# Kernel optimization log

Hardware: AMD Instinct MI355X
Metric: run time of the kernel (lower is better)

Reference implementation:

```python
import jax, jax.numpy as jnp
import numpy as np

VOCAB = 32000
DIM = 1024
DEPTH = 4
SEQ = 512
HEADS = 16
NMB = 4
MAXMEM = NMB * SEQ  # 2048
RAMP = 128
COEF = 1e-06
B = 4
DH = DIM // HEADS


def _ln(x, g, b):
    mu = jnp.mean(x, axis=-1, keepdims=True)
    v = jnp.mean((x - mu) ** 2, axis=-1, keepdims=True)
    return (x - mu) / jnp.sqrt(v + 1e-5) * g + b


def setup_inputs() -> dict:
    key = jax.random.key(0)
    ks = jax.random.split(key, 24)
    s = 0.02
    inp = {
        'tokens': jax.random.randint(ks[0], (B, SEQ), 0, VOCAB),
        'mems': jax.random.normal(ks[1], (DEPTH, B, MAXMEM, DIM), jnp.float32) * s,
        'times': jax.random.randint(ks[2], (DEPTH, MAXMEM), 0, 4096, dtype=jnp.int32),
        'token_emb': jax.random.normal(ks[3], (VOCAB, DIM), jnp.float32) * s,
        'expire_W': jax.random.normal(ks[4], (DEPTH, DIM), jnp.float32) * s,
        'expire_b': jnp.full((DEPTH,), -float(MAXMEM), jnp.float32),  # torch init constant
        'ln1_g': jnp.ones((DEPTH, DIM), jnp.float32),
        'ln1_b': jnp.zeros((DEPTH, DIM), jnp.float32),
        'Wq': jax.random.normal(ks[5], (DEPTH, DIM, DIM), jnp.float32) * s,
        'Wkv': jax.random.normal(ks[6], (DEPTH, DIM, 2 * DIM), jnp.float32) * s,
        'Wo': jax.random.normal(ks[7], (DEPTH, DIM, DIM), jnp.float32) * s,
        'bo': jnp.zeros((DEPTH, DIM), jnp.float32),
        'ln2_g': jnp.ones((DEPTH, DIM), jnp.float32),
        'ln2_b': jnp.zeros((DEPTH, DIM), jnp.float32),
        'W1': jax.random.normal(ks[8], (DEPTH, DIM, 4 * DIM), jnp.float32) * s,
        'b1': jnp.zeros((DEPTH, 4 * DIM), jnp.float32),
        'W2': jax.random.normal(ks[9], (DEPTH, 4 * DIM, DIM), jnp.float32) * s,
        'b2': jnp.zeros((DEPTH, DIM), jnp.float32),
        'logits_W': jax.random.normal(ks[10], (DIM, VOCAB), jnp.float32) * s,
        'logits_b': jnp.zeros((VOCAB,), jnp.float32),
    }
    return inp


def reference(tokens, mems, times, token_emb, expire_W, expire_b, ln1_g, ln1_b,
              Wq, Wkv, Wo, bo, ln2_g, ln2_b, W1, b1, W2, b2, logits_W, logits_b):
    n, M = SEQ, MAXMEM
    scale = DH ** -0.5
    x = token_emb[tokens]  # (B, n, DIM)
    # causal mask over concat(mem, x): query i may attend key j iff j <= i + M
    causal = jnp.triu(jnp.ones((n, M + n), bool), k=M + 1)  # True = masked
    aux = jnp.float32(0.0)
    new_mems, new_times = [], []
    tnew = jnp.arange(n - 1, -1, -1, dtype=times.dtype)
    for d in range(DEPTH):
        mem = mems[d]                       # (B, M, DIM)
        t = times[d].astype(jnp.float32)    # (M,)
        hidden = x
        # --- expire span: per-memory-slot soft retention mask ---
        exps = jax.nn.sigmoid(mem @ expire_W[d] + expire_b[d]) * M  # (B, M)
        r = exps[:, None, None, :] - t[None, None, None, :]          # (B,1,1,M)
        r = jnp.pad(r, ((0, 0), (0, 0), (0, 0), (0, n)), constant_values=1.0)
        emask = jnp.clip(r / RAMP + 1.0, 0.0, 1.0)                   # (B,1,1,M+n)
        # --- pre-norm causal attention over concat(mem, x_normed) ---
        xn = _ln(x, ln1_g[d], ln1_b[d])
        q = (xn @ Wq[d]).reshape(B, n, HEADS, DH).transpose(0, 2, 1, 3)
        ctx = jnp.concatenate([mem, xn], axis=1)                     # (B, M+n, DIM)
        kv = ctx @ Wkv[d]
        k = kv[..., :DIM].reshape(B, M + n, HEADS, DH).transpose(0, 2, 1, 3)
        v = kv[..., DIM:].reshape(B, M + n, HEADS, DH).transpose(0, 2, 1, 3)
        dots = jnp.einsum('bhid,bhjd->bhij', q, k) * scale
        dots = jnp.where(causal, -jnp.inf, dots)
        attn = jax.nn.softmax(dots, axis=-1) * emask
        out = jnp.einsum('bhij,bhjd->bhid', attn, v)
        out = out.transpose(0, 2, 1, 3).reshape(B, n, DIM)
        x = out @ Wo[d] + bo[d] + x
        # --- pre-norm FFN ---
        xn2 = _ln(x, ln2_g[d], ln2_b[d])
        x = jax.nn.gelu(xn2 @ W1[d] + b1[d], approximate=False) @ W2[d] + b2[d] + x
        aux = aux + (exps / SEQ).sum() * COEF
        # --- memory bookkeeping (detached) ---
        new_mems.append(jax.lax.stop_gradient(
            jnp.concatenate([mem, hidden], axis=1)[:, -M:]))
        new_times.append(jnp.concatenate([times[d] + n, tnew])[-M:])
    logits = x @ logits_W + logits_b
    return (logits, jnp.stack(new_mems), jnp.stack(new_times), aux)
```

## Files before the change

### kernel.cpp

```cpp
#include <hip/hip_runtime.h>
#include <cmath>

#define DIMC   1024
#define SEQC   512
#define BC     4
#define MC     2048
#define CTXC   2560
#define HEADSC 16
#define DHC    64
#define VOCABC 32000
#define MAXC   512

using short8 = __attribute__((ext_vector_type(8))) short;
using f32x4  = __attribute__((ext_vector_type(4))) float;
using u16x4  = __attribute__((ext_vector_type(4))) unsigned short;
using u16x8  = __attribute__((ext_vector_type(8))) unsigned short;

__device__ __forceinline__ unsigned short f2bf(float f) {
    unsigned u = __float_as_uint(f);
    unsigned r = (u + 0x7fffu + ((u >> 16) & 1u)) >> 16;
    return (unsigned short)r;
}

__device__ __forceinline__ void glds16(const unsigned short* g, char* l) {
    __builtin_amdgcn_global_load_lds(
        (const __attribute__((address_space(1))) void*)g,
        (__attribute__((address_space(3))) void*)l, 16, 0, 0);
}

__global__ __launch_bounds__(256) void embed_kernel(const int* __restrict__ tokens,
                                                    const float* __restrict__ emb,
                                                    float* __restrict__ x) {
    int row = blockIdx.x;
    int tok = tokens[row];
    const float4 v = *(const float4*)(emb + (size_t)tok * DIMC + threadIdx.x * 4);
    *(float4*)(x + (size_t)row * DIMC + threadIdx.x * 4) = v;
}

__global__ __launch_bounds__(256) void times_init_kernel(const int* __restrict__ times,
                                                         float* __restrict__ out_times,
                                                         float* __restrict__ aux) {
    int i = blockIdx.x * 256 + threadIdx.x;
    if (i == 0) aux[0] = 0.0f;
    if (i < 4 * MC) {
        int d = i >> 11, m = i & (MC - 1);
        out_times[i] = (m < MC - SEQC) ? (float)(times[d * MC + SEQC + m] + SEQC)
                                       : (float)(MC - 1 - m);
    }
}

#define PREP_MEM 8192
#define PREP_XC  10240
#define PREP_LN  12288
#define PREP_TOT 24576
__global__ __launch_bounds__(256) void prep_kernel(
    const float* __restrict__ mem_d, const float* __restrict__ x,
    const float* __restrict__ eW, const float* __restrict__ eb,
    float* __restrict__ exps, float* __restrict__ aux,
    unsigned short* __restrict__ mem_b, float* __restrict__ out_mems_d,
    const float* __restrict__ g1, const float* __restrict__ b1v,
    unsigned short* __restrict__ xn_b,
    const float* __restrict__ Wq, const float* __restrict__ Wkv,
    const float* __restrict__ Wo, const float* __restrict__ W1,
    const float* __restrict__ W2,
    unsigned short* __restrict__ wq_t, unsigned short* __restrict__ wkv_t,
    unsigned short* __restrict__ wo_t, unsigned short* __restrict__ w1_t,
    unsigned short* __restrict__ w2_t) {
    __shared__ float sh[1056];
    const int bid = blockIdx.x, tid = threadIdx.x;
    if (bid < PREP_MEM) {
        int row = bid;
        int m = row & 2047, b = row >> 11;
        const float4 v = *(const float4*)(mem_d + (size_t)row * DIMC + tid * 4);
        const float4 w = *(const float4*)(eW + tid * 4);
        float s = v.x * w.x + v.y * w.y + v.z * w.z + v.w * w.w;
        for (int off = 32; off; off >>= 1) s += __shfl_down(s, off, 64);
        int wid = tid >> 6, lane = tid & 63;
        if (lane == 0) sh[wid] = s;
        u16x4 o = { f2bf(v.x), f2bf(v.y), f2bf(v.z), f2bf(v.w) };
        *(u16x4*)(mem_b + (size_t)row * DIMC + tid * 4) = o;
        if (m >= SEQC)
            *(float4*)(out_mems_d + ((size_t)(b * MC + m - SEQC)) * DIMC + tid * 4) = v;
        __syncthreads();
        if (tid == 0) {
            float z = sh[0] + sh[1] + sh[2] + sh[3] + eb[0];
            float e = (float)MC / (1.0f + expf(-z));
            exps[row] = e;
            atomicAdd(aux, e * (1e-6f / (float)SEQC));
        }
    } else if (bid < PREP_XC) {
        int r = bid - PREP_MEM;
        int b = r >> 9, i = r & 511;
        const float4 v = *(const float4*)(x + (size_t)r * DIMC + tid * 4);
        *(float4*)(out_mems_d + ((size_t)(b * MC + MC - SEQC + i)) * DIMC + tid * 4) = v;
    } else if (bid < PREP_LN) {
        int row = bid - PREP_XC;
        const float4 v = *(const float4*)(x + (size_t)row * DIMC + tid * 4);
        float s = v.x + v.y + v.z + v.w;
        float q = v.x * v.x + v.y * v.y + v.z * v.z + v.w * v.w;
        for (int off = 32; off; off >>= 1) {
            s += __shfl_down(s, off, 64);
            q += __shfl_down(q, off, 64);
        }
        int wid = tid >> 6, lane = tid & 63;
        if (lane == 0) { sh[wid] = s; sh[4 + wid] = q; }
        __syncthreads();
        if (tid == 0) {
            float S = sh[0] + sh[1] + sh[2] + sh[3];
            float Q = sh[4] + sh[5] + sh[6] + sh[7];
            float mu = S / DIMC;
            float var = Q / DIMC - mu * mu;
            sh[8] = mu;
            sh[9] = rsqrtf(var + 1e-5f);
        }
        __syncthreads();
        float mu = sh[8], rstd = sh[9];
        const float4 gg = *(const float4*)(g1 + tid * 4);
        const float4 bb = *(const float4*)(b1v + tid * 4);
        u16x4 o = { f2bf((v.x - mu) * rstd * gg.x + bb.x),
                    f2bf((v.y - mu) * rstd * gg.y + bb.y),
                    f2bf((v.z - mu) * rstd * gg.z + bb.z),
                    f2bf((v.w - mu) * rstd * gg.w + bb.w) };
        *(u16x4*)(xn_b + (size_t)row * DIMC + tid * 4) = o;
    } else {
        int t = bid - PREP_LN;
        const float* W; unsigned short* Wt; int K, N, tx, ty;
        if (t < 1024)      { W = Wq;  Wt = wq_t;  K = 1024; N = 1024; tx = t & 31;  ty = t >> 5; }
        else if (t < 3072) { int u = t - 1024; W = Wkv; Wt = wkv_t; K = 1024; N = 2048; tx = u & 63;  ty = u >> 6; }
        else if (t < 4096) { int u = t - 3072; W = Wo;  Wt = wo_t;  K = 1024; N = 1024; tx = u & 31;  ty = u >> 5; }
        else if (t < 8192) { int u = t - 4096; W = W1;  Wt = w1_t;  K = 1024; N = 4096; tx = u & 127; ty = u >> 7; }
        else               { int u = t - 8192; W = W2;  Wt = w2_t;  K = 4096; N = 1024; tx = u & 31;  ty = u >> 5; }
        int n0 = tx * 32, k0 = ty * 32;
        int r = tid >> 3, c = (tid & 7) * 4;
        const float4 v = *(const float4*)(W + (size_t)(k0 + r) * N + n0 + c);
        sh[r * 33 + c] = v.x; sh[r * 33 + c + 1] = v.y;
        sh[r * 33 + c + 2] = v.z; sh[r * 33 + c + 3] = v.w;
        __syncthreads();
        u16x4 o = { f2bf(sh[(c + 0) * 33 + r]), f2bf(sh[(c + 1) * 33 + r]),
                    f2bf(sh[(c + 2) * 33 + r]), f2bf(sh[(c + 3) * 33 + r]) };
        *(u16x4*)(Wt + (size_t)(n0 + r) * K + k0 + c) = o;
    }
}

__global__ __launch_bounds__(64) void compact_kernel(
    const float* __restrict__ exps, const int* __restrict__ times_d,
    int* __restrict__ cidx, float* __restrict__ em_c, int* __restrict__ cnt) {
    int b = blockIdx.x, lane = threadIdx.x;
    int c = 0;
    for (int it = 0; it < 32; ++it) {
        int j = it * 64 + lane;
        float e = exps[b * MC + j];
        float rr = (e - (float)times_d[j]) * (1.0f / 128.0f) + 1.0f;
        float em = fminf(fmaxf(rr, 0.0f), 1.0f);
        unsigned long long mk = __ballot(em > 0.0f);
        int pos = c + __popcll(mk & ((1ull << lane) - 1ull));
        if (em > 0.0f) {
            cidx[b * 2048 + pos] = j;
            em_c[b * 2048 + pos] = em;
        }
        c += __popcll(mk);
    }
    int padded = (c + 63) & ~63;
    int fill_to = padded < MAXC ? MAXC : padded;
    for (int p = c + lane; p < fill_to; p += 64) {
        cidx[b * 2048 + p] = 0;
        em_c[b * 2048 + p] = 0.0f;
    }
    int tiles = padded >> 6;
    if (tiles > (MAXC >> 6)) tiles = MAXC >> 6;
    if (lane == 0) cnt[b] = tiles;
}

__global__ __launch_bounds__(256) void ln_kernel(const float* __restrict__ in,
                                                 const float* __restrict__ g,
                                                 const float* __restrict__ b,
                                                 unsigned short* __restrict__ outb) {
    int row = blockIdx.x;
    int tid = threadIdx.x;
    const float4 v = *(const float4*)(in + (size_t)row * DIMC + tid * 4);
    float s = v.x + v.y + v.z + v.w;
    float q = v.x * v.x + v.y * v.y + v.z * v.z + v.w * v.w;
    for (int off = 32; off; off >>= 1) {
        s += __shfl_down(s, off, 64);
        q += __shfl_down(q, off, 64);
    }
    __shared__ float ss[4], sq[4];
    int wid = tid >> 6, lane = tid & 63;
    if (lane == 0) { ss[wid] = s; sq[wid] = q; }
    __syncthreads();
    if (tid == 0) {
        float S = ss[0] + ss[1] + ss[2] + ss[3];
        float Q = sq[0] + sq[1] + sq[2] + sq[3];
        float mu = S / DIMC;
        float var = Q / DIMC - mu * mu;
        ss[0] = mu;
        sq[0] = rsqrtf(var + 1e-5f);
    }
    __syncthreads();
    float mu = ss[0], rstd = sq[0];
    const float4 gg = *(const float4*)(g + tid * 4);
    const float4 bb = *(const float4*)(b + tid * 4);
    u16x4 o = { f2bf((v.x - mu) * rstd * gg.x + bb.x),
                f2bf((v.y - mu) * rstd * gg.y + bb.y),
                f2bf((v.z - mu) * rstd * gg.z + bb.z),
                f2bf((v.w - mu) * rstd * gg.w + bb.w) };
    *(u16x4*)(outb + (size_t)row * DIMC + tid * 4) = o;
}

__global__ __launch_bounds__(256) void wt_kernel(const float* __restrict__ W,
                                                 unsigned short* __restrict__ Wt,
                                                 int K, int N) {
    __shared__ float t[32][33];
    int tid = threadIdx.x;
    int n0 = blockIdx.x * 32, k0 = blockIdx.y * 32;
    int r = tid >> 3, c = (tid & 7) * 4;
    const float4 v = *(const float4*)(W + (size_t)(k0 + r) * N + n0 + c);
    t[r][c] = v.x; t[r][c + 1] = v.y; t[r][c + 2] = v.z; t[r][c + 3] = v.w;
    __syncthreads();
    u16x4 o = { f2bf(t[c + 0][r]), f2bf(t[c + 1][r]),
                f2bf(t[c + 2][r]), f2bf(t[c + 3][r]) };
    *(u16x4*)(Wt + (size_t)(n0 + r) * K + k0 + c) = o;
}

template<int AMODE, bool BIAS, bool GELU, bool RES, int OMODE, int RT>
__device__ __forceinline__ void gemm_body(
    unsigned short* As, unsigned short* Bs,
    const unsigned short* __restrict__ A, const int* __restrict__ gidx,
    const unsigned short* __restrict__ Wt, const float* __restrict__ bias,
    const float* __restrict__ res, float* __restrict__ Cf,
    unsigned short* __restrict__ Cb, int K, int N, int bx, int by) {
    constexpr int MF = RT / 32;
    const int tid = threadIdx.x;
    const int lane = tid & 63, wave = tid >> 6;
    const int row0 = by * RT, col0 = bx * 128;

    const int seg = tid & 3;
    const int rr0 = tid >> 2;
    const unsigned short* arow[RT / 64];
    #pragma unroll
    for (int p = 0; p < RT / 64; ++p) {
        int r = row0 + p * 64 + rr0;
        if (AMODE == 2) {
            int b = r >> 9, slot = r & (MAXC - 1);
            arow[p] = A + ((size_t)(b * 2048 + gidx[b * 2048 + slot])) * K;
        } else {
            arow[p] = A + (size_t)r * K;
        }
        arow[p] += seg * 8;
    }
    const unsigned short* brow[2];
    #pragma unroll
    for (int p = 0; p < 2; ++p)
        brow[p] = Wt + (size_t)(col0 + p * 64 + rr0) * K + seg * 8;

    char* lA = (char*)As + (tid & 192) * 16;
    char* lB = (char*)Bs + (tid & 192) * 16;

    auto stage = [&](int k0, int q) {
        char* a = lA + q * (RT * 64);
        glds16(arow[0] + k0, a);
        if (RT == 128) glds16(arow[1] + k0, a + 4096);
        char* bp = lB + q * 8192;
        glds16(brow[0] + k0, bp);
        glds16(brow[1] + k0, bp + 4096);
    };

    f32x4 acc[MF][4] = {};

    const int wr = (wave >> 1) * (RT / 2), wc = (wave & 1) * 64;
    const int fr = lane & 15;
    const int k8 = (lane >> 4) * 8;

    stage(0, 0);
    int cur = 0;
    for (int k0 = 0; k0 < K; k0 += 32) {
        if (k0 + 32 < K) {
            stage(k0 + 32, cur ^ 1);
            if (RT == 128) asm volatile("s_waitcnt vmcnt(4)" ::: "memory");
            else           asm volatile("s_waitcnt vmcnt(3)" ::: "memory");
        } else {
            asm volatile("s_waitcnt vmcnt(0)" ::: "memory");
        }
        __builtin_amdgcn_s_barrier();
        __builtin_amdgcn_sched_barrier(0);
        const unsigned short* Ar = As + cur * (RT * 32) + (size_t)(wr + fr) * 32 + k8;
        const unsigned short* Br = Bs + cur * (128 * 32) + (size_t)(wc + fr) * 32 + k8;
        short8 a[MF], b[4];
        #pragma unroll
        for (int m = 0; m < MF; ++m) a[m] = *(const short8*)(Ar + m * 16 * 32);
        #pragma unroll
        for (int n = 0; n < 4; ++n) b[n] = *(const short8*)(Br + n * 16 * 32);
        #pragma unroll
        for (int m = 0; m < MF; ++m)
            #pragma unroll
            for (int n = 0; n < 4; ++n)
                acc[m][n] = __builtin_amdgcn_mfma_f32_16x16x32_bf16(a[m], b[n], acc[m][n], 0, 0, 0);
        __builtin_amdgcn_s_barrier();
        cur ^= 1;
    }

    const int orow = row0 + wr + (lane >> 4) * 4;
    const int ocol = col0 + wc + fr;
    if (OMODE >= 3) {
        #pragma unroll
        for (int n = 0; n < 4; ++n) {
            int c = ocol + n * 16;
            #pragma unroll
            for (int m = 0; m < MF; ++m) {
                int r0 = orow + m * 16;
                int b = r0 >> 9, i = r0 & 511;
                size_t addr = (OMODE == 3)
                    ? ((size_t)(b * 1024 + c)) * 512 + i
                    : ((size_t)(b * 1024 + c)) * MAXC + i;
                u16x4 o = { f2bf(acc[m][n][0]), f2bf(acc[m][n][1]),
                            f2bf(acc[m][n][2]), f2bf(acc[m][n][3]) };
                *(u16x4*)(Cb + addr) = o;
            }
        }
        return;
    }
    #pragma unroll
    for (int n = 0; n < 4; ++n) {
        int c = ocol + n * 16;
        float bv = BIAS ? bias[c] : 0.0f;
        #pragma unroll
        for (int m = 0; m < MF; ++m) {
            #pragma unroll
            for (int i = 0; i < 4; ++i) {
                int r0 = orow + m * 16 + i;
                size_t orr = r0;
                if (OMODE == 1) orr = (size_t)r0 + (size_t)(r0 >> 11) * 512;
                if (OMODE == 2) orr = (size_t)r0 + (size_t)(r0 >> 9) * 2048 + 2048;
                size_t idx = orr * N + c;
                float v = acc[m][n][i] + bv;
                if (GELU) v = 0.5f * v * (1.0f + erff(v * 0.70710678118f));
                if (RES) v += res[idx];
                if (Cf) Cf[idx] = v;
                if (Cb) Cb[idx] = f2bf(v);
            }
        }
    }
}

__global__ __launch_bounds__(256) void qkv_gemm_kernel(
    const unsigned short* __restrict__ xn_b, const unsigned short* __restrict__ mem_b,
    const unsigned short* __restrict__ wq_t, const unsigned short* __restrict__ wkv_t,
    const int* __restrict__ cidx, const int* __restrict__ cnt,
    unsigned short* __restrict__ qb, unsigned short* __restrict__ kvb,
    unsigned short* __restrict__ vTl, unsigned short* __restrict__ vTc) {
    __shared__ unsigned short As[2 * 128 * 32];
    __shared__ unsigned short Bs[2 * 128 * 32];
    int id = blockIdx.x;
    if (id < 128) {
        gemm_body<0, false, false, false, 0, 128>(As, Bs, xn_b, nullptr, wq_t,
            nullptr, nullptr, nullptr, qb, 1024, 1024, id & 7, id >> 3);
    } else if (id < 256) {
        id -= 128;
        gemm_body<0, false, false, false, 2, 128>(As, Bs, xn_b, nullptr, wkv_t,
            nullptr, nullptr, nullptr, kvb, 1024, 1024, id & 7, id >> 3);
    } else if (id < 768) {
        id -= 256;
        gemm_body<0, false, false, false, 1, 128>(As, Bs, mem_b, nullptr, wkv_t,
            nullptr, nullptr, nullptr, kvb, 1024, 1024, id & 7, id >> 3);
    } else if (id < 896) {
        id -= 768;
        gemm_body<0, false, false, false, 3, 128>(As, Bs, xn_b, nullptr,
            wkv_t + (size_t)1024 * 1024, nullptr, nullptr, nullptr, vTl,
            1024, 1024, id & 7, id >> 3);
    } else {
        id -= 896;
        int by = id >> 3;
        int b = (by * 64) >> 9, slot0 = (by * 64) & (MAXC - 1);
        if (slot0 >= cnt[b] * 64) return;
        gemm_body<2, false, false, false, 4, 64>(As, Bs, mem_b, cidx,
            wkv_t + (size_t)1024 * 1024, nullptr, nullptr, nullptr, vTc,
            1024, 1024, id & 7, by);
    }
}

__global__ __launch_bounds__(256) void gemm64_kernel(
    const unsigned short* __restrict__ A, const unsigned short* __restrict__ Wt,
    const float* __restrict__ bias, const float* __restrict__ res,
    float* __restrict__ Cf, unsigned short* __restrict__ Cb, int K) {
    __shared__ unsigned short As[2 * 64 * 32];
    __shared__ unsigned short Bs[2 * 128 * 32];
    gemm_body<0, true, false, true, 0, 64>(As, Bs, A, nullptr, Wt, bias, res,
        Cf, Cb, K, 1024, blockIdx.x, blockIdx.y);
}

__global__ __launch_bounds__(256) void ffn1_kernel(
    const unsigned short* __restrict__ A, const unsigned short* __restrict__ Wt,
    const float* __restrict__ bias, unsigned short* __restrict__ Cb) {
    __shared__ unsigned short As[2 * 128 * 32];
    __shared__ unsigned short Bs[2 * 128 * 32];
    gemm_body<0, true, true, false, 0, 128>(As, Bs, A, nullptr, Wt, bias, nullptr,
        nullptr, Cb, 1024, 4096, blockIdx.x, blockIdx.y);
}

__global__ __launch_bounds__(512, 2) void logits_kernel(
    const unsigned short* __restrict__ A, const unsigned short* __restrict__ Wt,
    const float* __restrict__ bias, float* __restrict__ Cf) {
    __shared__ unsigned short As[2 * 256 * 32];
    __shared__ unsigned short Bs[2 * 256 * 32];
    const int L = blockIdx.x;
    const int wid = (L & 7) * 125 + (L >> 3);
    const int ct = wid / 8, rt = wid & 7;
    const int row0 = rt * 256, col0 = ct * 256;
    const int tid = threadIdx.x;
    const int lane = tid & 63, wave = tid >> 6;

    const int seg = tid & 3;
    const int rr0 = tid >> 2;
    const unsigned short* arow[2];
    const unsigned short* brow[2];
    #pragma unroll
    for (int p = 0; p < 2; ++p) {
        arow[p] = A + (size_t)(row0 + p * 128 + rr0) * 1024 + seg * 8;
        brow[p] = Wt + (size_t)(col0 + p * 128 + rr0) * 1024 + seg * 8;
    }
    char* lA = (char*)As + (tid & 448) * 16;
    char* lB = (char*)Bs + (tid & 448) * 16;

    auto stage = [&](int k0, int q) {
        char* a = lA + q * 16384;
        char* bp = lB + q * 16384;
        glds16(arow[0] + k0, a);
        glds16(arow[1] + k0, a + 8192);
        glds16(brow[0] + k0, bp);
        glds16(brow[1] + k0, bp + 8192);
    };

    f32x4 acc[8][4] = {};
    const int wr = (wave >> 2) * 128, wc = (wave & 3) * 64;
    const int fr = lane & 15;
    const int k8 = (lane >> 4) * 8;

    stage(0, 0);
    int cur = 0;
    for (int k0 = 0; k0 < 1024; k0 += 32) {
        if (k0 + 32 < 1024) {
            stage(k0 + 32, cur ^ 1);
            asm volatile("s_waitcnt vmcnt(4)" ::: "memory");
        } else {
            asm volatile("s_waitcnt vmcnt(0)" ::: "memory");
        }
        __builtin_amdgcn_s_barrier();
        __builtin_amdgcn_sched_barrier(0);
        const unsigned short* Ar = As + cur * 8192 + (size_t)(wr + fr) * 32 + k8;
        const unsigned short* Br = Bs + cur * 8192 + (size_t)(wc + fr) * 32 + k8;
        short8 a[8], b[4];
        #pragma unroll
        for (int m = 0; m < 8; ++m) a[m] = *(const short8*)(Ar + m * 16 * 32);
        #pragma unroll
        for (int n = 0; n < 4; ++n) b[n] = *(const short8*)(Br + n * 16 * 32);
        #pragma unroll
        for (int m = 0; m < 8; ++m)
            #pragma unroll
            for (int n = 0; n < 4; ++n)
                acc[m][n] = __builtin_amdgcn_mfma_f32_16x16x32_bf16(a[m], b[n], acc[m][n], 0, 0, 0);
        __builtin_amdgcn_s_barrier();
        cur ^= 1;
    }

    const int orow = row0 + wr + (lane >> 4) * 4;
    const int ocol = col0 + wc + fr;
    #pragma unroll
    for (int n = 0; n < 4; ++n) {
        int c = ocol + n * 16;
        float bv = bias[c];
        #pragma unroll
        for (int m = 0; m < 8; ++m) {
            #pragma unroll
            for (int i = 0; i < 4; ++i)
                Cf[(size_t)(orow + m * 16 + i) * VOCABC + c] = acc[m][n][i] + bv;
        }
    }
}

__global__ __launch_bounds__(512) void attn_mfma_kernel(
    const unsigned short* __restrict__ qb,
    const unsigned short* __restrict__ kvb,
    const unsigned short* __restrict__ vTl,
    const unsigned short* __restrict__ vTc,
    const int* __restrict__ cidx,
    const float* __restrict__ em_c,
    const int* __restrict__ cnt,
    unsigned short* __restrict__ outb) {
    __shared__ unsigned short K_s[2][64 * 64];
    __shared__ unsigned short V_s[2][64 * 64];
    __shared__ unsigned short p_s[8][16][72];
    __shared__ float em_s[64];
    const int tid = threadIdx.x;
    const int lane = tid & 63, wave = tid >> 6;
    const int L = blockIdx.x;
    const int ix = L >> 3;
    const int qt = ix & 3;
    const int gidx = (L & 7) * 8 + (ix >> 2);
    const int h = gidx & 15, b = gidx >> 4;
    const int fr = lane & 15, g = lane >> 4;
    const int gq = qt * 128 + wave * 16;

    short8 aq[2];
    {
        const unsigned short* qp = qb + ((size_t)(b * SEQC + gq + fr)) * DIMC + h * DHC + g * 8;
        aq[0] = *(const short8*)qp;
        aq[1] = *(const short8*)(qp + 32);
    }

    const int sr = tid >> 3, ss = tid & 7;
    const int sw = (ss ^ (sr & 7)) * 8;
    const int wbase = (tid & 448) * 16;

    f32x4 acc_o[4] = {};
    float m_q = -1e30f, l_q = 0.0f;

    const int nlt = 2 * (qt + 1);
    const int nt = 32 + nlt;

    auto stage12 = [&](int t, int q) {
        const int jbase = t * 64;
        glds16(kvb + ((size_t)(b * CTXC + jbase + sr)) * 1024 + h * DHC + sw,
               (char*)K_s[q] + wbase);
        if (t >= 32)
            glds16(vTl + ((size_t)(b * 1024 + h * DHC + sr)) * 512 + (jbase - 2048) + sw,
                   (char*)V_s[q] + wbase);
    };

    stage12(0, 0);
    asm volatile("s_waitcnt vmcnt(0)" ::: "memory");
    __builtin_amdgcn_s_barrier();
    int cur = 0;
    for (int t = 0; t < nt; ++t) {
        if (t + 1 < nt) stage12(t + 1, cur ^ 1);
        if (t + 1 >= nt)      asm volatile("s_waitcnt vmcnt(0)" ::: "memory");
        else if (t >= 31)     asm volatile("s_waitcnt vmcnt(2)" ::: "memory");
        else                  asm volatile("s_waitcnt vmcnt(1)" ::: "memory");
        __builtin_amdgcn_s_barrier();
        __builtin_amdgcn_sched_barrier(0);

        const bool live = (t < 32) || ((t - 32) * 64 <= gq + 15);
        if (live) {
            f32x4 sT[4] = {};
            #pragma unroll
            for (int ks = 0; ks < 2; ++ks)
                #pragma unroll
                for (int mf = 0; mf < 4; ++mf) {
                    int row = mf * 16 + fr, sg = (ks * 4 + g) ^ (row & 7);
                    short8 kk = *(const short8*)((const char*)K_s[cur] + row * 128 + sg * 16);
                    sT[mf] = __builtin_amdgcn_mfma_f32_16x16x32_bf16(kk, aq[ks], sT[mf], 0, 0, 0);
                }

            if (t < 32) {
                float mx = sT[0][0];
                #pragma unroll
                for (int mf = 0; mf < 4; ++mf)
                    #pragma unroll
                    for (int i = 0; i < 4; ++i) mx = fmaxf(mx, sT[mf][i]);
                mx *= 0.125f;
                mx = fmaxf(mx, __shfl_xor(mx, 16, 64));
                mx = fmaxf(mx, __shfl_xor(mx, 32, 64));
                float mnew = fmaxf(m_q, mx);
                float fs = __expf(m_q - mnew);
                m_q = mnew;
                float ps = 0.0f;
                #pragma unroll
                for (int mf = 0; mf < 4; ++mf)
                    #pragma unroll
                    for (int i = 0; i < 4; ++i)
                        ps += __expf(sT[mf][i] * 0.125f - mnew);
                ps += __shfl_xor(ps, 16, 64);
                ps += __shfl_xor(ps, 32, 64);
                l_q = l_q * fs + ps;
            } else {
                const int lt = t - 32;
                const int kq = gq + fr - lt * 64;
                float sv[4][4];
                #pragma unroll
                for (int mf = 0; mf < 4; ++mf)
                    #pragma unroll
                    for (int i = 0; i < 4; ++i) {
                        int kl = mf * 16 + g * 4 + i;
                        sv[mf][i] = (kl <= kq) ? sT[mf][i] * 0.125f : -1e30f;
                    }
                float mx = sv[0][0];
                #pragma unroll
                for (int mf = 0; mf < 4; ++mf)
                    #pragma unroll
                    for (int i = 0; i < 4; ++i) mx = fmaxf(mx, sv[mf][i]);
                mx = fmaxf(mx, __shfl_xor(mx, 16, 64));
                mx = fmaxf(mx, __shfl_xor(mx, 32, 64));
                float mnew = fmaxf(m_q, mx);
                float fs = __expf(m_q - mnew);
                m_q = mnew;
                float ps = 0.0f;
                #pragma unroll
                for (int mf = 0; mf < 4; ++mf)
                    #pragma unroll
                    for (int i = 0; i < 4; ++i) {
                        float pe = __expf(sv[mf][i] - mnew);
                        ps += pe;
                        p_s[wave][fr][mf * 16 + g * 4 + i] = f2bf(pe);
                    }
                ps += __shfl_xor(ps, 16, 64);
                ps += __shfl_xor(ps, 32, 64);
                l_q = l_q * fs + ps;
                float fsr[4];
                #pragma unroll
                for (int i = 0; i < 4; ++i) fsr[i] = __shfl(fs, g * 4 + i, 64);
                #pragma unroll
                for (int n = 0; n < 4; ++n)
                    #pragma unroll
                    for (int i = 0; i < 4; ++i) acc_o[n][i] *= fsr[i];
                asm volatile("s_waitcnt lgkmcnt(0)" ::: "memory");
                #pragma unroll
                for (int ks = 0; ks < 2; ++ks) {
                    short8 ap = *(const short8*)&p_s[wave][fr][ks * 32 + g * 8];
                    #pragma unroll
                    for (int n = 0; n < 4; ++n) {
                        int row = n * 16 + fr, sg = (ks * 4 + g) ^ (row & 7);
                        short8 bv = *(const short8*)((const char*)V_s[cur] + row * 128 + sg * 16);
                        acc_o[n] = __builtin_amdgcn_mfma_f32_16x16x32_bf16(ap, bv, acc_o[n], 0, 0, 0);
                    }
                }
            }
        }
        __builtin_amdgcn_s_barrier();
        cur ^= 1;
    }

    const int nct = cnt[b];
    for (int ct = 0; ct < nct; ++ct) {
        __syncthreads();
        {
            int row = cidx[b * 2048 + ct * 64 + sr];
            glds16(kvb + ((size_t)(b * CTXC + row)) * 1024 + h * DHC + sw,
                   (char*)K_s[0] + wbase);
            glds16(vTc + ((size_t)(b * 1024 + h * DHC + sr)) * MAXC + ct * 64 + sw,
                   (char*)V_s[0] + wbase);
        }
        if (tid < 64) em_s[tid] = em_c[b * 2048 + ct * 64 + tid];
        __syncthreads();
        f32x4 sT[4] = {};
        #pragma unroll
        for (int ks = 0; ks < 2; ++ks)
            #pragma unroll
            for (int mf = 0; mf < 4; ++mf) {
                int row = mf * 16 + fr, sg = (ks * 4 + g) ^ (row & 7);
                short8 kk = *(const short8*)((const char*)K_s[0] + row * 128 + sg * 16);
                sT[mf] = __builtin_amdgcn_mfma_f32_16x16x32_bf16(kk, aq[ks], sT[mf], 0, 0, 0);
            }
        #pragma unroll
        for (int mf = 0; mf < 4; ++mf)
            #pragma unroll
            for (int i = 0; i < 4; ++i) {
                int key = mf * 16 + g * 4 + i;
                float pe = __expf(sT[mf][i] * 0.125f - m_q) * em_s[key];
                p_s[wave][fr][key] = f2bf(pe);
            }
        asm volatile("s_waitcnt lgkmcnt(0)" ::: "memory");
        #pragma unroll
        for (int ks = 0; ks < 2; ++ks) {
            short8 ap = *(const short8*)&p_s[wave][fr][ks * 32 + g * 8];
            #pragma unroll
            for (int n = 0; n < 4; ++n) {
                int row = n * 16 + fr, sg = (ks * 4 + g) ^ (row & 7);
                short8 bv = *(const short8*)((const char*)V_s[0] + row * 128 + sg * 16);
                acc_o[n] = __builtin_amdgcn_mfma_f32_16x16x32_bf16(ap, bv, acc_o[n], 0, 0, 0);
            }
        }
    }

    float linv = 1.0f / l_q;
    float invr[4];
    #pragma unroll
    for (int i = 0; i < 4; ++i) invr[i] = __shfl(linv, g * 4 + i, 64);
    #pragma unroll
    for (int n = 0; n < 4; ++n) {
        #pragma unroll
        for (int i = 0; i < 4; ++i) {
            size_t idx = ((size_t)(b * SEQC + gq + g * 4 + i)) * DIMC + h * DHC + n * 16 + fr;
            outb[idx] = f2bf(acc_o[n][i] * invr[i]);
        }
    }
}

__global__ void aux_write_kernel(const float* __restrict__ aux, float* __restrict__ dst) {
    dst[0] = aux[0];
}

extern "C" void kernel_launch(void* const* d_in, const int* in_sizes, int n_in,
                              void* d_out, int out_size, void* d_ws, size_t ws_size,
                              hipStream_t stream) {
    const int*   tokens    = (const int*)d_in[0];
    const float* mems      = (const float*)d_in[1];
    const int*   times     = (const int*)d_in[2];
    const float* token_emb = (const float*)d_in[3];
    const float* expire_W  = (const float*)d_in[4];
    const float* expire_b  = (const float*)d_in[5];
    const float* ln1_g     = (const float*)d_in[6];
    const float* ln1_b     = (const float*)d_in[7];
    const float* Wq        = (const float*)d_in[8];
    const float* Wkv       = (const float*)d_in[9];
    const float* Wo        = (const float*)d_in[10];
    const float* bo        = (const float*)d_in[11];
    const float* ln2_g     = (const float*)d_in[12];
    const float* ln2_b     = (const float*)d_in[13];
    const float* W1        = (const float*)d_in[14];
    const float* b1        = (const float*)d_in[15];
    const float* W2        = (const float*)d_in[16];
    const float* b2        = (const float*)d_in[17];
    const float* logits_W  = (const float*)d_in[18];
    const float* logits_b  = (const float*)d_in[19];

    float* out = (float*)d_out;
    float* ws  = (float*)d_ws;

    float* x = ws;
    unsigned short* qb_b  = (unsigned short*)(ws + 2097152);
    unsigned short* kv_b  = (unsigned short*)(ws + 3145728);
    unsigned short* vTl   = (unsigned short*)(ws + 8388608);
    unsigned short* vTc   = (unsigned short*)(ws + 9437184);
    unsigned short* xn_b  = (unsigned short*)(ws + 10485760);
    unsigned short* attn_b= (unsigned short*)(ws + 11534336);
    unsigned short* ffn_b = (unsigned short*)(ws + 12582912);
    unsigned short* mem_b = (unsigned short*)(ws + 16777216);
    unsigned short* x_b   = (unsigned short*)(ws + 20971520);
    unsigned short* wq_t  = (unsigned short*)(ws + 22020096);
    unsigned short* wkv_t = (unsigned short*)(ws + 22544384);
    unsigned short* wo_t  = (unsigned short*)(ws + 23592960);
    unsigned short* w1_t  = (unsigned short*)(ws + 24117248);
    unsigned short* w2_t  = (unsigned short*)(ws + 26214400);
    float* exps = ws + 28311552;
    float* aux  = ws + 28319744;
    int*   cidx = (int*)(ws + 28319760);
    float* em_c = ws + 28327952;
    int*   cnt  = (int*)(ws + 28336144);
    unsigned short* lw_t = (unsigned short*)(ws + 2097152);

    float* out_logits = out;
    float* out_mems   = out + 65536000;
    float* out_times  = out + 99090432;

    embed_kernel<<<BC * SEQC, 256, 0, stream>>>(tokens, token_emb, x);
    times_init_kernel<<<32, 256, 0, stream>>>(times, out_times, aux);

    for (int d = 0; d < 4; ++d) {
        const float* mem_d = mems + (size_t)d * BC * MC * DIMC;
        prep_kernel<<<PREP_TOT, 256, 0, stream>>>(
            mem_d, x, expire_W + d * DIMC, expire_b + d, exps, aux,
            mem_b, out_mems + (size_t)d * BC * MC * DIMC,
            ln1_g + d * DIMC, ln1_b + d * DIMC, xn_b,
            Wq + (size_t)d * DIMC * DIMC, Wkv + (size_t)d * DIMC * 2 * DIMC,
            Wo + (size_t)d * DIMC * DIMC, W1 + (size_t)d * DIMC * 4 * DIMC,
            W2 + (size_t)d * 4 * DIMC * DIMC,
            wq_t, wkv_t, wo_t, w1_t, w2_t);
        compact_kernel<<<BC, 64, 0, stream>>>(exps, times + d * MC, cidx, em_c, cnt);
        qkv_gemm_kernel<<<1152, 256, 0, stream>>>(xn_b, mem_b, wq_t, wkv_t,
                                                  cidx, cnt, qb_b, kv_b, vTl, vTc);
        attn_mfma_kernel<<<256, 512, 0, stream>>>(
            qb_b, kv_b, vTl, vTc, cidx, em_c, cnt, attn_b);
        gemm64_kernel<<<dim3(8, 32), 256, 0, stream>>>(
            attn_b, wo_t, bo + d * DIMC, x, x, nullptr, DIMC);
        ln_kernel<<<BC * SEQC, 256, 0, stream>>>(x, ln2_g + d * DIMC, ln2_b + d * DIMC, xn_b);
        ffn1_kernel<<<dim3(32, 16), 256, 0, stream>>>(xn_b, w1_t, b1 + d * 4 * DIMC, ffn_b);
        if (d < 3) {
            gemm64_kernel<<<dim3(8, 32), 256, 0, stream>>>(
                ffn_b, w2_t, b2 + d * DIMC, x, x, nullptr, 4 * DIMC);
        } else {
            gemm64_kernel<<<dim3(8, 32), 256, 0, stream>>>(
                ffn_b, w2_t, b2 + d * DIMC, x, nullptr, x_b, 4 * DIMC);
        }
    }

    wt_kernel<<<dim3(1000, 32), 256, 0, stream>>>(logits_W, lw_t, DIMC, VOCABC);
    logits_kernel<<<1000, 512, 0, stream>>>(x_b, lw_t, logits_b, out_logits);
    aux_write_kernel<<<1, 1, 0, stream>>>(aux, out + 99098624);
}
```

Baseline: 1.727 ms.

## Split attention into 64-query blocks of 4 waves with 512 workgroups

The attention kernel now uses 256-thread blocks covering 64 query rows each, launched as 512 blocks instead of 256 blocks of 512 threads covering 128 rows. Each thread stages two rows per tile, and the wait counts are adjusted to match. The per-wave liveness skip is dropped because every wave in a block now needs the same number of local tiles (33+qt). The aim is finer causal load balancing, since per-block tile counts now grow in steps of one instead of two, and more blocks to fill the GPU. The cost is that the 2048-key memory K tiles and the compacted tiles are loaded twice as often across the grid.

```diff
diff --git a/kernel.cpp b/kernel.cpp
--- a/kernel.cpp
+++ b/kernel.cpp
@@ -477,7 +477,7 @@
     }
 }
 
-__global__ __launch_bounds__(512) void attn_mfma_kernel(
+__global__ __launch_bounds__(256) void attn_mfma_kernel(
     const unsigned short* __restrict__ qb,
     const unsigned short* __restrict__ kvb,
     const unsigned short* __restrict__ vTl,
@@ -488,17 +488,17 @@
     unsigned short* __restrict__ outb) {
     __shared__ unsigned short K_s[2][64 * 64];
     __shared__ unsigned short V_s[2][64 * 64];
-    __shared__ unsigned short p_s[8][16][72];
+    __shared__ unsigned short p_s[4][16][72];
     __shared__ float em_s[64];
     const int tid = threadIdx.x;
     const int lane = tid & 63, wave = tid >> 6;
     const int L = blockIdx.x;
     const int ix = L >> 3;
-    const int qt = ix & 3;
-    const int gidx = (L & 7) * 8 + (ix >> 2);
+    const int qt = ix & 7;
+    const int gidx = (L & 7) * 8 + (ix >> 3);
     const int h = gidx & 15, b = gidx >> 4;
     const int fr = lane & 15, g = lane >> 4;
-    const int gq = qt * 128 + wave * 16;
+    const int gq = qt * 64 + wave * 16;
 
     short8 aq[2];
     {
@@ -509,21 +509,24 @@
 
     const int sr = tid >> 3, ss = tid & 7;
     const int sw = (ss ^ (sr & 7)) * 8;
-    const int wbase = (tid & 448) * 16;
+    const int wbase = (tid & 192) * 16;
 
     f32x4 acc_o[4] = {};
     float m_q = -1e30f, l_q = 0.0f;
 
-    const int nlt = 2 * (qt + 1);
-    const int nt = 32 + nlt;
+    const int nt = 33 + qt;
 
     auto stage12 = [&](int t, int q) {
         const int jbase = t * 64;
-        glds16(kvb + ((size_t)(b * CTXC + jbase + sr)) * 1024 + h * DHC + sw,
-               (char*)K_s[q] + wbase);
-        if (t >= 32)
-            glds16(vTl + ((size_t)(b * 1024 + h * DHC + sr)) * 512 + (jbase - 2048) + sw,
-                   (char*)V_s[q] + wbase);
+        #pragma unroll
+        for (int p = 0; p < 2; ++p) {
+            int r = sr + p * 32;
+            glds16(kvb + ((size_t)(b * CTXC + jbase + r)) * 1024 + h * DHC + sw,
+                   (char*)K_s[q] + wbase + p * 4096);
+            if (t >= 32)
+                glds16(vTl + ((size_t)(b * 1024 + h * DHC + r)) * 512 + (jbase - 2048) + sw,
+                       (char*)V_s[q] + wbase + p * 4096);
+        }
     };
 
     stage12(0, 0);
@@ -533,94 +536,91 @@
     for (int t = 0; t < nt; ++t) {
         if (t + 1 < nt) stage12(t + 1, cur ^ 1);
         if (t + 1 >= nt)      asm volatile("s_waitcnt vmcnt(0)" ::: "memory");
-        else if (t >= 31)     asm volatile("s_waitcnt vmcnt(2)" ::: "memory");
-        else                  asm volatile("s_waitcnt vmcnt(1)" ::: "memory");
+        else if (t + 1 >= 32) asm volatile("s_waitcnt vmcnt(4)" ::: "memory");
+        else                  asm volatile("s_waitcnt vmcnt(2)" ::: "memory");
         __builtin_amdgcn_s_barrier();
         __builtin_amdgcn_sched_barrier(0);
 
-        const bool live = (t < 32) || ((t - 32) * 64 <= gq + 15);
-        if (live) {
-            f32x4 sT[4] = {};
-            #pragma unroll
-            for (int ks = 0; ks < 2; ++ks)
+        f32x4 sT[4] = {};
+        #pragma unroll
+        for (int ks = 0; ks < 2; ++ks)
+            #pragma unroll
+            for (int mf = 0; mf < 4; ++mf) {
+                int row = mf * 16 + fr, sg = (ks * 4 + g) ^ (row & 7);
+                short8 kk = *(const short8*)((const char*)K_s[cur] + row * 128 + sg * 16);
+                sT[mf] = __builtin_amdgcn_mfma_f32_16x16x32_bf16(kk, aq[ks], sT[mf], 0, 0, 0);
+            }
+
+        if (t < 32) {
+            float mx = sT[0][0];
+            #pragma unroll
+            for (int mf = 0; mf < 4; ++mf)
                 #pragma unroll
-                for (int mf = 0; mf < 4; ++mf) {
-                    int row = mf * 16 + fr, sg = (ks * 4 + g) ^ (row & 7);
-                    short8 kk = *(const short8*)((const char*)K_s[cur] + row * 128 + sg * 16);
-                    sT[mf] = __builtin_amdgcn_mfma_f32_16x16x32_bf16(kk, aq[ks], sT[mf], 0, 0, 0);
+                for (int i = 0; i < 4; ++i) mx = fmaxf(mx, sT[mf][i]);
+            mx *= 0.125f;
+            mx = fmaxf(mx, __shfl_xor(mx, 16, 64));
+            mx = fmaxf(mx, __shfl_xor(mx, 32, 64));
+            float mnew = fmaxf(m_q, mx);
+            float fs = __expf(m_q - mnew);
+            m_q = mnew;
+            float ps = 0.0f;
+            #pragma unroll
+            for (int mf = 0; mf < 4; ++mf)
+                #pragma unroll
+                for (int i = 0; i < 4; ++i)
+                    ps += __expf(sT[mf][i] * 0.125f - mnew);
+            ps += __shfl_xor(ps, 16, 64);
+            ps += __shfl_xor(ps, 32, 64);
+            l_q = l_q * fs + ps;
+        } else {
+            const int lt = t - 32;
+            const int kq = gq + fr - lt * 64;
+            float sv[4][4];
+            #pragma unroll
+            for (int mf = 0; mf < 4; ++mf)
+                #pragma unroll
+                for (int i = 0; i < 4; ++i) {
+                    int kl = mf * 16 + g * 4 + i;
+                    sv[mf][i] = (kl <= kq) ? sT[mf][i] * 0.125f : -1e30f;
                 }
-
-            if (t < 32) {
-                float mx = sT[0][0];
+            float mx = sv[0][0];
+            #pragma unroll
+            for (int mf = 0; mf < 4; ++mf)
                 #pragma unroll
-                for (int mf = 0; mf < 4; ++mf)
-                    #pragma unroll
-                    for (int i = 0; i < 4; ++i) mx = fmaxf(mx, sT[mf][i]);
-                mx *= 0.125f;
-                mx = fmaxf(mx, __shfl_xor(mx, 16, 64));
-                mx = fmaxf(mx, __shfl_xor(mx, 32, 64));
-                float mnew = fmaxf(m_q, mx);
-                float fs = __expf(m_q - mnew);
-                m_q = mnew;
-                float ps = 0.0f;
+                for (int i = 0; i < 4; ++i) mx = fmaxf(mx, sv[mf][i]);
+            mx = fmaxf(mx, __shfl_xor(mx, 16, 64));
+            mx = fmaxf(mx, __shfl_xor(mx, 32, 64));
+            float mnew = fmaxf(m_q, mx);
+            float fs = __expf(m_q - mnew);
+            m_q = mnew;
+            float ps = 0.0f;
+            #pragma unroll
+            for (int mf = 0; mf < 4; ++mf)
                 #pragma unroll
-                for (int mf = 0; mf < 4; ++mf)
-                    #pragma unroll
-                    for (int i = 0; i < 4; ++i)
-                        ps += __expf(sT[mf][i] * 0.125f - mnew);
-                ps += __shfl_xor(ps, 16, 64);
-                ps += __shfl_xor(ps, 32, 64);
-                l_q = l_q * fs + ps;
-            } else {
-                const int lt = t - 32;
-                const int kq = gq + fr - lt * 64;
-                float sv[4][4];
+                for (int i = 0; i < 4; ++i) {
+                    float pe = __expf(sv[mf][i] - mnew);
+                    ps += pe;
+                    p_s[wave][fr][mf * 16 + g * 4 + i] = f2bf(pe);
+                }
+            ps += __shfl_xor(ps, 16, 64);
+            ps += __shfl_xor(ps, 32, 64);
+            l_q = l_q * fs + ps;
+            float fsr[4];
+            #pragma unroll
+            for (int i = 0; i < 4; ++i) fsr[i] = __shfl(fs, g * 4 + i, 64);
+            #pragma unroll
+            for (int n = 0; n < 4; ++n)
                 #pragma unroll
-                for (int mf = 0; mf < 4; ++mf)
-                    #pragma unroll
-                    for (int i = 0; i < 4; ++i) {
-                        int kl = mf * 16 + g * 4 + i;
-                        sv[mf][i] = (kl <= kq) ? sT[mf][i] * 0.125f : -1e30f;
-                    }
-                float mx = sv[0][0];
+                for (int i = 0; i < 4; ++i) acc_o[n][i] *= fsr[i];
+            asm volatile("s_waitcnt lgkmcnt(0)" ::: "memory");
+            #pragma unroll
+            for (int ks = 0; ks < 2; ++ks) {
+                short8 ap = *(const short8*)&p_s[wave][fr][ks * 32 + g * 8];
                 #pragma unroll
-                for (int mf = 0; mf < 4; ++mf)
-                    #pragma unroll
-                    for (int i = 0; i < 4; ++i) mx = fmaxf(mx, sv[mf][i]);
-                mx = fmaxf(mx, __shfl_xor(mx, 16, 64));
-                mx = fmaxf(mx, __shfl_xor(mx, 32, 64));
-                float mnew = fmaxf(m_q, mx);
-                float fs = __expf(m_q - mnew);
-                m_q = mnew;
-                float ps = 0.0f;
-                #pragma unroll
-                for (int mf = 0; mf < 4; ++mf)
-                    #pragma unroll
-                    for (int i = 0; i < 4; ++i) {
-                        float pe = __expf(sv[mf][i] - mnew);
-                        ps += pe;
-                        p_s[wave][fr][mf * 16 + g * 4 + i] = f2bf(pe);
-                    }
-                ps += __shfl_xor(ps, 16, 64);
-                ps += __shfl_xor(ps, 32, 64);
-                l_q = l_q * fs + ps;
-                float fsr[4];
-                #pragma unroll
-                for (int i = 0; i < 4; ++i) fsr[i] = __shfl(fs, g * 4 + i, 64);
-                #pragma unroll
-                for (int n = 0; n < 4; ++n)
-                    #pragma unroll
-                    for (int i = 0; i < 4; ++i) acc_o[n][i] *= fsr[i];
-                asm volatile("s_waitcnt lgkmcnt(0)" ::: "memory");
-                #pragma unroll
-                for (int ks = 0; ks < 2; ++ks) {
-                    short8 ap = *(const short8*)&p_s[wave][fr][ks * 32 + g * 8];
-                    #pragma unroll
-                    for (int n = 0; n < 4; ++n) {
-                        int row = n * 16 + fr, sg = (ks * 4 + g) ^ (row & 7);
-                        short8 bv = *(const short8*)((const char*)V_s[cur] + row * 128 + sg * 16);
-                        acc_o[n] = __builtin_amdgcn_mfma_f32_16x16x32_bf16(ap, bv, acc_o[n], 0, 0, 0);
-                    }
+                for (int n = 0; n < 4; ++n) {
+                    int row = n * 16 + fr, sg = (ks * 4 + g) ^ (row & 7);
+                    short8 bv = *(const short8*)((const char*)V_s[cur] + row * 128 + sg * 16);
+                    acc_o[n] = __builtin_amdgcn_mfma_f32_16x16x32_bf16(ap, bv, acc_o[n], 0, 0, 0);
                 }
             }
         }
@@ -631,12 +631,14 @@
     const int nct = cnt[b];
     for (int ct = 0; ct < nct; ++ct) {
         __syncthreads();
-        {
-            int row = cidx[b * 2048 + ct * 64 + sr];
+        #pragma unroll
+        for (int p = 0; p < 2; ++p) {
+            int r = sr + p * 32;
+            int row = cidx[b * 2048 + ct * 64 + r];
             glds16(kvb + ((size_t)(b * CTXC + row)) * 1024 + h * DHC + sw,
-                   (char*)K_s[0] + wbase);
-            glds16(vTc + ((size_t)(b * 1024 + h * DHC + sr)) * MAXC + ct * 64 + sw,
-                   (char*)V_s[0] + wbase);
+                   (char*)K_s[0] + wbase + p * 4096);
+            glds16(vTc + ((size_t)(b * 1024 + h * DHC + r)) * MAXC + ct * 64 + sw,
+                   (char*)V_s[0] + wbase + p * 4096);
         }
         if (tid < 64) em_s[tid] = em_c[b * 2048 + ct * 64 + tid];
         __syncthreads();
@@ -757,7 +759,7 @@
         compact_kernel<<<BC, 64, 0, stream>>>(exps, times + d * MC, cidx, em_c, cnt);
         qkv_gemm_kernel<<<1152, 256, 0, stream>>>(xn_b, mem_b, wq_t, wkv_t,
                                                   cidx, cnt, qb_b, kv_b, vTl, vTc);
-        attn_mfma_kernel<<<256, 512, 0, stream>>>(
+        attn_mfma_kernel<<<512, 256, 0, stream>>>(
             qb_b, kv_b, vTl, vTc, cidx, em_c, cnt, attn_b);
         gemm64_kernel<<<dim3(8, 32), 256, 0, stream>>>(
             attn_b, wo_t, bo + d * DIMC, x, x, nullptr, DIMC);
```

Measured after the change: 1.727 ms. Within noise of the previous version (+0.0%).
